# Performance work log

Measured on AMD Instinct MI355X. Metric: run time of the kernel, lower is better.

The kernel has to match this reference:

```python
import jax, jax.numpy as jnp
import numpy as np

N = 8192          # number of nodes
F_IN = 256        # in_features
F_OUT = 128       # out_features


def setup_inputs() -> dict:
    key = jax.random.key(0)
    k1, k2, k3, k4 = jax.random.split(key, 4)
    input = jax.random.normal(k1, (N, F_IN), dtype=jnp.float32)
    adj = jax.random.uniform(k2, (N, N), dtype=jnp.float32)
    stdv = 1.0 / np.sqrt(F_OUT)
    weight = jax.random.uniform(k3, (F_IN, F_OUT), dtype=jnp.float32, minval=-stdv, maxval=stdv)
    bias = jax.random.uniform(k4, (F_OUT,), dtype=jnp.float32, minval=-stdv, maxval=stdv)
    return {"input": input, "adj": adj, "weight": weight, "bias": bias}


def reference(input, adj, weight, bias):
    # support = X @ W  [N, F_OUT]
    support = jnp.matmul(input, weight)
    # Subgraph block decomposition over a node partition is exactly A @ support:
    # block (k,i) computes adj[S_k][:, S_i] @ support[S_i] scatter-added into rows S_k.
    output = jnp.matmul(adj, support)  # [N, F_OUT]
    return output + bias
```

## Files before the change

kernel.cpp:

```cpp
#include <hip/hip_runtime.h>
#include <hip/hip_bf16.h>

#define N_NODES 8192
#define F_IN 256
#define F_OUT 128

#define SPLITK 4
#define KQ (N_NODES / SPLITK)
#define BK 64
#define NT (KQ / BK)
#define ABYTES 16384
#define BBYTES 16384
#define BUFB (ABYTES + BBYTES)

typedef __attribute__((ext_vector_type(4))) float f32x4;
typedef __attribute__((ext_vector_type(8))) short bf16x8;

static __device__ __forceinline__ short bfr(float x) {
    __hip_bfloat16 h = __float2bfloat16(x);
    union { __hip_bfloat16 h; short s; } u; u.h = h;
    return u.s;
}

static __device__ __forceinline__ void gload16(const void* g, void* l) {
    __builtin_amdgcn_global_load_lds(
        (const __attribute__((address_space(1))) unsigned int*)g,
        (__attribute__((address_space(3))) unsigned int*)l, 16, 0, 0);
}

__global__ __launch_bounds__(256) void support_kernel(
        const float* __restrict__ X, const float* __restrict__ W,
        unsigned short* __restrict__ supT) {
    __shared__ float Xs[32][68];
    __shared__ float Ws[64][128];
    const int t = threadIdx.x;
    const int n0 = blockIdx.x * 32;
    const int tc = t & 31;
    const int tr = t >> 5;
    float acc[4][4];
    #pragma unroll
    for (int i = 0; i < 4; ++i)
        #pragma unroll
        for (int j = 0; j < 4; ++j) acc[i][j] = 0.f;

    for (int k0 = 0; k0 < F_IN; k0 += 64) {
        __syncthreads();
        {
            const int r = t >> 3, kc = (t & 7) * 8;
            const float* src = X + (size_t)(n0 + r) * F_IN + k0 + kc;
            f32x4 v0 = *(const f32x4*)src;
            f32x4 v1 = *(const f32x4*)(src + 4);
            *(f32x4*)&Xs[r][kc]     = v0;
            *(f32x4*)&Xs[r][kc + 4] = v1;
        }
        {
            const int col = t & 127, kb = t >> 7;
            #pragma unroll
            for (int i = 0; i < 32; ++i) {
                const int k = kb + i * 2;
                Ws[k][col] = W[(size_t)(k0 + k) * F_OUT + col];
            }
        }
        __syncthreads();
        #pragma unroll 8
        for (int k = 0; k < 64; ++k) {
            const f32x4 b = *(const f32x4*)&Ws[k][tc * 4];
            float a[4];
            #pragma unroll
            for (int i = 0; i < 4; ++i) a[i] = Xs[tr * 4 + i][k];
            #pragma unroll
            for (int i = 0; i < 4; ++i) {
                acc[i][0] += a[i] * b.x; acc[i][1] += a[i] * b.y;
                acc[i][2] += a[i] * b.z; acc[i][3] += a[i] * b.w;
            }
        }
    }
    #pragma unroll
    for (int j = 0; j < 4; ++j) {
        const int col = tc * 4 + j;
        #pragma unroll
        for (int i = 0; i < 4; ++i) {
            supT[(size_t)col * N_NODES + n0 + tr * 4 + i] =
                (unsigned short)bfr(acc[i][j]);
        }
    }
}

__global__ __launch_bounds__(512, 4) void gcn_kernel(
        const float* __restrict__ adj, const unsigned short* __restrict__ supT,
        float* __restrict__ part) {
    __shared__ char lds[2 * BUFB];
    const int t = threadIdx.x;
    const int l = t & 63;
    const int w = t >> 6;
    const int rb = blockIdx.x & 127;
    const int h = blockIdx.x >> 7;
    const int n0 = rb * 64;
    const int k0 = h * KQ;

    const int rA0 = 8 * w + (l >> 4);
    const int rA1 = rA0 + 4;
    const char* gA0 = (const char*)adj
        + ((size_t)(n0 + rA0) * N_NODES + k0) * 4 + (((l & 15) ^ (rA0 & 15)) * 16);
    const char* gA1 = (const char*)adj
        + ((size_t)(n0 + rA1) * N_NODES + k0) * 4 + (((l & 15) ^ (rA1 & 15)) * 16);
    const char* gB0 = (const char*)supT
        + ((size_t)(16 * w + (l >> 3)) * N_NODES + k0) * 2 + (((l & 7) ^ (l >> 3)) * 16);
    const char* gB1 = gB0 + (size_t)8 * N_NODES * 2;

    const int a_d0 = w * 2048;
    const int a_d1 = a_d0 + 1024;
    const int b_d0 = ABYTES + w * 2048;
    const int b_d1 = b_d0 + 1024;

    const int wm = w >> 2, wn = w & 3;
    const int aoff0 = (wm * 32 + (l & 15)) * 256;
    const int aoff1 = aoff0 + 16 * 256;
    const int akey = l & 15;
    const int ac0 = (l >> 4) * 2;
    const int boff0 = ABYTES + (wn * 32 + (l & 15)) * 128;
    const int boff1 = boff0 + 16 * 128;
    const int bkey = l & 7;
    const int cb0 = l >> 4;

    f32x4 acc00 = {0.f,0.f,0.f,0.f}, acc01 = {0.f,0.f,0.f,0.f};
    f32x4 acc10 = {0.f,0.f,0.f,0.f}, acc11 = {0.f,0.f,0.f,0.f};

#define STAGE(BUF) { \
    char* bb = &lds[(BUF) * BUFB]; \
    gload16(gA0, bb + a_d0); \
    gload16(gA1, bb + a_d1); \
    gload16(gB0, bb + b_d0); \
    gload16(gB1, bb + b_d1); \
    gA0 += 256; gA1 += 256; gB0 += 128; gB1 += 128; }

#define FENCE_BARRIER() { \
    asm volatile("s_waitcnt vmcnt(0)" ::: "memory"); \
    __builtin_amdgcn_sched_barrier(0); \
    __builtin_amdgcn_s_barrier(); \
    __builtin_amdgcn_sched_barrier(0); }

    STAGE(0);
    FENCE_BARRIER();

    for (int tt = 0; tt < NT; ++tt) {
        if (tt + 1 < NT) STAGE((tt + 1) & 1);

        const char* buf = &lds[(tt & 1) * BUFB];
        #pragma unroll
        for (int ks = 0; ks < 2; ++ks) {
            const int ca = ks * 8 + ac0;
            f32x4 a0lo = *(const f32x4*)(buf + aoff0 + (((ca    ) ^ akey) * 16));
            f32x4 a0hi = *(const f32x4*)(buf + aoff0 + (((ca + 1) ^ akey) * 16));
            f32x4 a1lo = *(const f32x4*)(buf + aoff1 + (((ca    ) ^ akey) * 16));
            f32x4 a1hi = *(const f32x4*)(buf + aoff1 + (((ca + 1) ^ akey) * 16));
            const int cb = ks * 4 + cb0;
            bf16x8 b0 = *(const bf16x8*)(buf + boff0 + ((cb ^ bkey) * 16));
            bf16x8 b1 = *(const bf16x8*)(buf + boff1 + ((cb ^ bkey) * 16));
            bf16x8 am0, am1;
            am0[0] = bfr(a0lo.x); am0[1] = bfr(a0lo.y);
            am0[2] = bfr(a0lo.z); am0[3] = bfr(a0lo.w);
            am0[4] = bfr(a0hi.x); am0[5] = bfr(a0hi.y);
            am0[6] = bfr(a0hi.z); am0[7] = bfr(a0hi.w);
            am1[0] = bfr(a1lo.x); am1[1] = bfr(a1lo.y);
            am1[2] = bfr(a1lo.z); am1[3] = bfr(a1lo.w);
            am1[4] = bfr(a1hi.x); am1[5] = bfr(a1hi.y);
            am1[6] = bfr(a1hi.z); am1[7] = bfr(a1hi.w);
            acc00 = __builtin_amdgcn_mfma_f32_16x16x32_bf16(am0, b0, acc00, 0, 0, 0);
            acc01 = __builtin_amdgcn_mfma_f32_16x16x32_bf16(am0, b1, acc01, 0, 0, 0);
            acc10 = __builtin_amdgcn_mfma_f32_16x16x32_bf16(am1, b0, acc10, 0, 0, 0);
            acc11 = __builtin_amdgcn_mfma_f32_16x16x32_bf16(am1, b1, acc11, 0, 0, 0);
        }
        FENCE_BARRIER();
    }
#undef STAGE
#undef FENCE_BARRIER

    float* p = part + (size_t)h * N_NODES * F_OUT;
    const int col = wn * 32 + (l & 15);
    const int row0 = n0 + wm * 32 + (l >> 4) * 4;
    #pragma unroll
    for (int i = 0; i < 4; ++i) {
        float* o0 = p + (size_t)(row0 + i) * F_OUT + col;
        float* o1 = p + (size_t)(row0 + i + 16) * F_OUT + col;
        o0[0]  = acc00[i];
        o0[16] = acc01[i];
        o1[0]  = acc10[i];
        o1[16] = acc11[i];
    }
}

__global__ __launch_bounds__(256) void add_kernel(
        const float* __restrict__ part, const float* __restrict__ bias,
        float* __restrict__ out) {
    const int i = blockIdx.x * 256 + threadIdx.x;
    const size_t e = (size_t)i * 8;
    const size_t ps = (size_t)N_NODES * F_OUT;
    f32x4 s0 = *(const f32x4*)(part + e);
    f32x4 s1 = *(const f32x4*)(part + e + 4);
    #pragma unroll
    for (int h = 1; h < SPLITK; ++h) {
        s0 += *(const f32x4*)(part + h * ps + e);
        s1 += *(const f32x4*)(part + h * ps + e + 4);
    }
    const int fb = (i & 15) * 8;
    s0 += *(const f32x4*)(bias + fb);
    s1 += *(const f32x4*)(bias + fb + 4);
    *(f32x4*)(out + e)     = s0;
    *(f32x4*)(out + e + 4) = s1;
}

extern "C" void kernel_launch(void* const* d_in, const int* in_sizes, int n_in,
                              void* d_out, int out_size, void* d_ws, size_t ws_size,
                              hipStream_t stream) {
    const float* input  = (const float*)d_in[0];
    const float* adj    = (const float*)d_in[1];
    const float* weight = (const float*)d_in[2];
    const float* bias   = (const float*)d_in[3];
    float* out = (float*)d_out;
    unsigned short* supT = (unsigned short*)d_ws;
    float* part = (float*)((char*)d_ws + (4u << 20));

    support_kernel<<<N_NODES / 32, 256, 0, stream>>>(input, weight, supT);
    gcn_kernel<<<128 * SPLITK, 512, 0, stream>>>(adj, supT, part);
    add_kernel<<<(N_NODES * F_OUT) / (256 * 8), 256, 0, stream>>>(part, bias, out);
}
```

Measured before the change: 83.66 us.

## Deepen gcn_kernel pipeline to four LDS buffers with smaller K tiles

Halves the K tile to 32 and replaces the double-buffered load/compute loop with a 4-stage ring of LDS buffers. Three stages are prefetched and partial vmcnt waits are used, so global loads stay in flight across iterations instead of draining with vmcnt(0) every tile. The aim is to hide adj streaming latency in this memory-bound GEMM. In exchange there are twice as many barriers per K, and the swizzle and index math has to be redone for the new tile size.

Result: slower. 99.75 us (+19.2%).

```diff
diff --git a/kernel.cpp b/kernel.cpp
--- a/kernel.cpp
+++ b/kernel.cpp
@@ -7,11 +7,12 @@
 
 #define SPLITK 4
 #define KQ (N_NODES / SPLITK)
-#define BK 64
+#define BK 32
 #define NT (KQ / BK)
-#define ABYTES 16384
-#define BBYTES 16384
+#define ABYTES 8192
+#define BBYTES 8192
 #define BUFB (ABYTES + BBYTES)
+#define NBUF 4
 
 typedef __attribute__((ext_vector_type(4))) float f32x4;
 typedef __attribute__((ext_vector_type(8))) short bf16x8;
@@ -89,7 +90,7 @@
 __global__ __launch_bounds__(512, 4) void gcn_kernel(
         const float* __restrict__ adj, const unsigned short* __restrict__ supT,
         float* __restrict__ part) {
-    __shared__ char lds[2 * BUFB];
+    __shared__ char lds[NBUF * BUFB];
     const int t = threadIdx.x;
     const int l = t & 63;
     const int w = t >> 6;
@@ -98,83 +99,74 @@
     const int n0 = rb * 64;
     const int k0 = h * KQ;
 
-    const int rA0 = 8 * w + (l >> 4);
-    const int rA1 = rA0 + 4;
-    const char* gA0 = (const char*)adj
-        + ((size_t)(n0 + rA0) * N_NODES + k0) * 4 + (((l & 15) ^ (rA0 & 15)) * 16);
-    const char* gA1 = (const char*)adj
-        + ((size_t)(n0 + rA1) * N_NODES + k0) * 4 + (((l & 15) ^ (rA1 & 15)) * 16);
-    const char* gB0 = (const char*)supT
-        + ((size_t)(16 * w + (l >> 3)) * N_NODES + k0) * 2 + (((l & 7) ^ (l >> 3)) * 16);
-    const char* gB1 = gB0 + (size_t)8 * N_NODES * 2;
-
-    const int a_d0 = w * 2048;
-    const int a_d1 = a_d0 + 1024;
-    const int b_d0 = ABYTES + w * 2048;
-    const int b_d1 = b_d0 + 1024;
+    const int rA = 8 * w + (l >> 3);
+    const char* gA = (const char*)adj
+        + ((size_t)(n0 + rA) * N_NODES + k0) * 4
+        + (((l & 7) ^ ((l >> 3) & 7)) * 16);
+    const int fB = 16 * w + (l >> 2);
+    const char* gB = (const char*)supT
+        + ((size_t)fB * N_NODES + k0) * 2
+        + (((l & 3) ^ ((l >> 3) & 3)) * 16);
+
+    const int a_d = w * 1024;
+    const int b_d = ABYTES + w * 1024;
 
     const int wm = w >> 2, wn = w & 3;
-    const int aoff0 = (wm * 32 + (l & 15)) * 256;
-    const int aoff1 = aoff0 + 16 * 256;
-    const int akey = l & 15;
-    const int ac0 = (l >> 4) * 2;
-    const int boff0 = ABYTES + (wn * 32 + (l & 15)) * 128;
-    const int boff1 = boff0 + 16 * 128;
-    const int bkey = l & 7;
-    const int cb0 = l >> 4;
+    const int aoff0 = (wm * 32 + (l & 15)) * 128;
+    const int aoff1 = aoff0 + 16 * 128;
+    const int akey = l & 7;
+    const int boff0 = ABYTES + (wn * 32 + (l & 15)) * 64;
+    const int boff1 = boff0 + 16 * 64;
+    const int bkey = (l >> 1) & 3;
+    const int j = l >> 4;
 
     f32x4 acc00 = {0.f,0.f,0.f,0.f}, acc01 = {0.f,0.f,0.f,0.f};
     f32x4 acc10 = {0.f,0.f,0.f,0.f}, acc11 = {0.f,0.f,0.f,0.f};
 
 #define STAGE(BUF) { \
     char* bb = &lds[(BUF) * BUFB]; \
-    gload16(gA0, bb + a_d0); \
-    gload16(gA1, bb + a_d1); \
-    gload16(gB0, bb + b_d0); \
-    gload16(gB1, bb + b_d1); \
-    gA0 += 256; gA1 += 256; gB0 += 128; gB1 += 128; }
-
-#define FENCE_BARRIER() { \
-    asm volatile("s_waitcnt vmcnt(0)" ::: "memory"); \
+    gload16(gA, bb + a_d); \
+    gload16(gB, bb + b_d); \
+    gA += 128; gB += 64; }
+
+#define BODY(TT, WAITIMM, DO_STAGE) { \
+    asm volatile("s_waitcnt vmcnt(" WAITIMM ")" ::: "memory"); \
     __builtin_amdgcn_sched_barrier(0); \
     __builtin_amdgcn_s_barrier(); \
-    __builtin_amdgcn_sched_barrier(0); }
-
-    STAGE(0);
-    FENCE_BARRIER();
-
-    for (int tt = 0; tt < NT; ++tt) {
-        if (tt + 1 < NT) STAGE((tt + 1) & 1);
-
-        const char* buf = &lds[(tt & 1) * BUFB];
-        #pragma unroll
-        for (int ks = 0; ks < 2; ++ks) {
-            const int ca = ks * 8 + ac0;
-            f32x4 a0lo = *(const f32x4*)(buf + aoff0 + (((ca    ) ^ akey) * 16));
-            f32x4 a0hi = *(const f32x4*)(buf + aoff0 + (((ca + 1) ^ akey) * 16));
-            f32x4 a1lo = *(const f32x4*)(buf + aoff1 + (((ca    ) ^ akey) * 16));
-            f32x4 a1hi = *(const f32x4*)(buf + aoff1 + (((ca + 1) ^ akey) * 16));
-            const int cb = ks * 4 + cb0;
-            bf16x8 b0 = *(const bf16x8*)(buf + boff0 + ((cb ^ bkey) * 16));
-            bf16x8 b1 = *(const bf16x8*)(buf + boff1 + ((cb ^ bkey) * 16));
-            bf16x8 am0, am1;
-            am0[0] = bfr(a0lo.x); am0[1] = bfr(a0lo.y);
-            am0[2] = bfr(a0lo.z); am0[3] = bfr(a0lo.w);
-            am0[4] = bfr(a0hi.x); am0[5] = bfr(a0hi.y);
-            am0[6] = bfr(a0hi.z); am0[7] = bfr(a0hi.w);
-            am1[0] = bfr(a1lo.x); am1[1] = bfr(a1lo.y);
-            am1[2] = bfr(a1lo.z); am1[3] = bfr(a1lo.w);
-            am1[4] = bfr(a1hi.x); am1[5] = bfr(a1hi.y);
-            am1[6] = bfr(a1hi.z); am1[7] = bfr(a1hi.w);
-            acc00 = __builtin_amdgcn_mfma_f32_16x16x32_bf16(am0, b0, acc00, 0, 0, 0);
-            acc01 = __builtin_amdgcn_mfma_f32_16x16x32_bf16(am0, b1, acc01, 0, 0, 0);
-            acc10 = __builtin_amdgcn_mfma_f32_16x16x32_bf16(am1, b0, acc10, 0, 0, 0);
-            acc11 = __builtin_amdgcn_mfma_f32_16x16x32_bf16(am1, b1, acc11, 0, 0, 0);
-        }
-        FENCE_BARRIER();
-    }
+    __builtin_amdgcn_sched_barrier(0); \
+    if (DO_STAGE) STAGE(((TT) + 3) & (NBUF - 1)); \
+    const char* buf = &lds[((TT) & (NBUF - 1)) * BUFB]; \
+    f32x4 a0lo = *(const f32x4*)(buf + aoff0 + (((2*j    ) ^ akey) * 16)); \
+    f32x4 a0hi = *(const f32x4*)(buf + aoff0 + (((2*j + 1) ^ akey) * 16)); \
+    f32x4 a1lo = *(const f32x4*)(buf + aoff1 + (((2*j    ) ^ akey) * 16)); \
+    f32x4 a1hi = *(const f32x4*)(buf + aoff1 + (((2*j + 1) ^ akey) * 16)); \
+    bf16x8 b0 = *(const bf16x8*)(buf + boff0 + ((j ^ bkey) * 16)); \
+    bf16x8 b1 = *(const bf16x8*)(buf + boff1 + ((j ^ bkey) * 16)); \
+    bf16x8 am0, am1; \
+    am0[0] = bfr(a0lo.x); am0[1] = bfr(a0lo.y); \
+    am0[2] = bfr(a0lo.z); am0[3] = bfr(a0lo.w); \
+    am0[4] = bfr(a0hi.x); am0[5] = bfr(a0hi.y); \
+    am0[6] = bfr(a0hi.z); am0[7] = bfr(a0hi.w); \
+    am1[0] = bfr(a1lo.x); am1[1] = bfr(a1lo.y); \
+    am1[2] = bfr(a1lo.z); am1[3] = bfr(a1lo.w); \
+    am1[4] = bfr(a1hi.x); am1[5] = bfr(a1hi.y); \
+    am1[6] = bfr(a1hi.z); am1[7] = bfr(a1hi.w); \
+    acc00 = __builtin_amdgcn_mfma_f32_16x16x32_bf16(am0, b0, acc00, 0, 0, 0); \
+    acc01 = __builtin_amdgcn_mfma_f32_16x16x32_bf16(am0, b1, acc01, 0, 0, 0); \
+    acc10 = __builtin_amdgcn_mfma_f32_16x16x32_bf16(am1, b0, acc10, 0, 0, 0); \
+    acc11 = __builtin_amdgcn_mfma_f32_16x16x32_bf16(am1, b1, acc11, 0, 0, 0); }
+
+    STAGE(0); STAGE(1); STAGE(2);
+
+    for (int tt = 0; tt < NT - 3; ++tt) {
+        BODY(tt, "4", 1);
+    }
+    BODY(NT - 3, "4", 0);
+    BODY(NT - 2, "2", 0);
+    BODY(NT - 1, "0", 0);
+
+#undef BODY
 #undef STAGE
-#undef FENCE_BARRIER
 
     float* p = part + (size_t)h * N_NODES * F_OUT;
     const int col = wn * 32 + (l & 15);
```

## Triple-buffer adj tiles and prefetch two stages ahead in GCN kernel

Applied to the files above, without the earlier changes.

Moves the adj (A) operand to a three-buffer LDS ring and keeps supT (B) double-buffered, so A loads are issued two iterations ahead. Each iteration now waits with a partial vmcnt and a single barrier instead of a full drain at the end of the loop. This is meant to hide the latency of the large fp32 adj stream behind MFMA work. It raises LDS use from 64KB to 80KB per block via dynamic shared memory, which may reduce occupancy, and it depends on the vmcnt counts matching the issue order.

New measurement: 87.23 us. 1.04x slower.

```diff
diff --git a/kernel.cpp b/kernel.cpp
--- a/kernel.cpp
+++ b/kernel.cpp
@@ -11,7 +11,7 @@
 #define NT (KQ / BK)
 #define ABYTES 16384
 #define BBYTES 16384
-#define BUFB (ABYTES + BBYTES)
+#define LDS_TOTAL (3 * ABYTES + 2 * BBYTES)
 
 typedef __attribute__((ext_vector_type(4))) float f32x4;
 typedef __attribute__((ext_vector_type(8))) short bf16x8;
@@ -89,7 +89,7 @@
 __global__ __launch_bounds__(512, 4) void gcn_kernel(
         const float* __restrict__ adj, const unsigned short* __restrict__ supT,
         float* __restrict__ part) {
-    __shared__ char lds[2 * BUFB];
+    extern __shared__ char lds[];
     const int t = threadIdx.x;
     const int l = t & 63;
     const int w = t >> 6;
@@ -110,7 +110,7 @@
 
     const int a_d0 = w * 2048;
     const int a_d1 = a_d0 + 1024;
-    const int b_d0 = ABYTES + w * 2048;
+    const int b_d0 = w * 2048;
     const int b_d1 = b_d0 + 1024;
 
     const int wm = w >> 2, wn = w & 3;
@@ -118,7 +118,7 @@
     const int aoff1 = aoff0 + 16 * 256;
     const int akey = l & 15;
     const int ac0 = (l >> 4) * 2;
-    const int boff0 = ABYTES + (wn * 32 + (l & 15)) * 128;
+    const int boff0 = (wn * 32 + (l & 15)) * 128;
     const int boff1 = boff0 + 16 * 128;
     const int bkey = l & 7;
     const int cb0 = l >> 4;
@@ -126,37 +126,46 @@
     f32x4 acc00 = {0.f,0.f,0.f,0.f}, acc01 = {0.f,0.f,0.f,0.f};
     f32x4 acc10 = {0.f,0.f,0.f,0.f}, acc11 = {0.f,0.f,0.f,0.f};
 
-#define STAGE(BUF) { \
-    char* bb = &lds[(BUF) * BUFB]; \
+#define STAGE_A(OFF) { \
+    char* bb = &lds[OFF]; \
     gload16(gA0, bb + a_d0); \
     gload16(gA1, bb + a_d1); \
+    gA0 += 256; gA1 += 256; }
+
+#define STAGE_B(OFF) { \
+    char* bb = &lds[3 * ABYTES + (OFF)]; \
     gload16(gB0, bb + b_d0); \
     gload16(gB1, bb + b_d1); \
-    gA0 += 256; gA1 += 256; gB0 += 128; gB1 += 128; }
-
-#define FENCE_BARRIER() { \
-    asm volatile("s_waitcnt vmcnt(0)" ::: "memory"); \
-    __builtin_amdgcn_sched_barrier(0); \
-    __builtin_amdgcn_s_barrier(); \
-    __builtin_amdgcn_sched_barrier(0); }
-
-    STAGE(0);
-    FENCE_BARRIER();
-
+    gB0 += 128; gB1 += 128; }
+
+    STAGE_B(0);
+    STAGE_A(0);
+    STAGE_A(ABYTES);
+
+    int ai = 0;
+    int bi = 0;
     for (int tt = 0; tt < NT; ++tt) {
-        if (tt + 1 < NT) STAGE((tt + 1) & 1);
-
-        const char* buf = &lds[(tt & 1) * BUFB];
+        if (tt < NT - 1) asm volatile("s_waitcnt vmcnt(2)" ::: "memory");
+        else             asm volatile("s_waitcnt vmcnt(0)" ::: "memory");
+        __builtin_amdgcn_sched_barrier(0);
+        __builtin_amdgcn_s_barrier();
+        __builtin_amdgcn_sched_barrier(0);
+
+        if (tt < NT - 1) STAGE_B((bi ^ 1) * BBYTES);
+        if (tt < NT - 2) { const int as = ai ? ai - 1 : 2; STAGE_A(as * ABYTES); }
+
+        const char* abuf = &lds[ai * ABYTES];
+        const char* bbuf = &lds[3 * ABYTES + bi * BBYTES];
         #pragma unroll
         for (int ks = 0; ks < 2; ++ks) {
             const int ca = ks * 8 + ac0;
-            f32x4 a0lo = *(const f32x4*)(buf + aoff0 + (((ca    ) ^ akey) * 16));
-            f32x4 a0hi = *(const f32x4*)(buf + aoff0 + (((ca + 1) ^ akey) * 16));
-            f32x4 a1lo = *(const f32x4*)(buf + aoff1 + (((ca    ) ^ akey) * 16));
-            f32x4 a1hi = *(const f32x4*)(buf + aoff1 + (((ca + 1) ^ akey) * 16));
+            f32x4 a0lo = *(const f32x4*)(abuf + aoff0 + (((ca    ) ^ akey) * 16));
+            f32x4 a0hi = *(const f32x4*)(abuf + aoff0 + (((ca + 1) ^ akey) * 16));
+            f32x4 a1lo = *(const f32x4*)(abuf + aoff1 + (((ca    ) ^ akey) * 16));
+            f32x4 a1hi = *(const f32x4*)(abuf + aoff1 + (((ca + 1) ^ akey) * 16));
             const int cb = ks * 4 + cb0;
-            bf16x8 b0 = *(const bf16x8*)(buf + boff0 + ((cb ^ bkey) * 16));
-            bf16x8 b1 = *(const bf16x8*)(buf + boff1 + ((cb ^ bkey) * 16));
+            bf16x8 b0 = *(const bf16x8*)(bbuf + boff0 + ((cb ^ bkey) * 16));
+            bf16x8 b1 = *(const bf16x8*)(bbuf + boff1 + ((cb ^ bkey) * 16));
             bf16x8 am0, am1;
             am0[0] = bfr(a0lo.x); am0[1] = bfr(a0lo.y);
             am0[2] = bfr(a0lo.z); am0[3] = bfr(a0lo.w);
@@ -171,10 +180,11 @@
             acc10 = __builtin_amdgcn_mfma_f32_16x16x32_bf16(am1, b0, acc10, 0, 0, 0);
             acc11 = __builtin_amdgcn_mfma_f32_16x16x32_bf16(am1, b1, acc11, 0, 0, 0);
         }
-        FENCE_BARRIER();
-    }
-#undef STAGE
-#undef FENCE_BARRIER
+        ai = (ai == 2) ? 0 : ai + 1;
+        bi ^= 1;
+    }
+#undef STAGE_A
+#undef STAGE_B
 
     float* p = part + (size_t)h * N_NODES * F_OUT;
     const int col = wn * 32 + (l & 15);
@@ -221,7 +231,11 @@
     unsigned short* supT = (unsigned short*)d_ws;
     float* part = (float*)((char*)d_ws + (4u << 20));
 
+    (void)hipFuncSetAttribute((const void*)gcn_kernel,
+                              hipFuncAttributeMaxDynamicSharedMemorySize,
+                              LDS_TOTAL);
+
     support_kernel<<<N_NODES / 32, 256, 0, stream>>>(input, weight, supT);
-    gcn_kernel<<<128 * SPLITK, 512, 0, stream>>>(adj, supT, part);
+    gcn_kernel<<<128 * SPLITK, 512, LDS_TOTAL, stream>>>(adj, supT, part);
     add_kernel<<<(N_NODES * F_OUT) / (256 * 8), 256, 0, stream>>>(part, bias, out);
 }
```

## Fuse split-K reduction and bias into GEMM via atomics; use packed bf16 convert

Applied to the files above, without the earlier changes.

Removes the separate add_kernel and the partial-sum workspace. Each split-K block now atomically adds its tile into a zeroed output, and the h==0 block also adds the bias. The fp32-to-bf16 conversion of adj tiles switches from per-element bfr calls to the packed v_cvt_pk_bf16_f32 instruction, halving the conversion instructions in the inner loop. In exchange it adds a memset, lets the float summation order vary between runs, and relies on atomic throughput to the output.

Measured after the change: 77.73 us. 7.1% less time.

```diff
diff --git a/kernel.cpp b/kernel.cpp
--- a/kernel.cpp
+++ b/kernel.cpp
@@ -15,6 +15,7 @@
 
 typedef __attribute__((ext_vector_type(4))) float f32x4;
 typedef __attribute__((ext_vector_type(8))) short bf16x8;
+typedef __attribute__((ext_vector_type(4))) unsigned int u32x4;
 
 static __device__ __forceinline__ short bfr(float x) {
     __hip_bfloat16 h = __float2bfloat16(x);
@@ -88,7 +89,7 @@
 
 __global__ __launch_bounds__(512, 4) void gcn_kernel(
         const float* __restrict__ adj, const unsigned short* __restrict__ supT,
-        float* __restrict__ part) {
+        const float* __restrict__ bias, float* __restrict__ out) {
     __shared__ char lds[2 * BUFB];
     const int t = threadIdx.x;
     const int l = t & 63;
@@ -125,6 +126,9 @@
 
     f32x4 acc00 = {0.f,0.f,0.f,0.f}, acc01 = {0.f,0.f,0.f,0.f};
     f32x4 acc10 = {0.f,0.f,0.f,0.f}, acc11 = {0.f,0.f,0.f,0.f};
+
+#define PK(dst, a, b) \
+    asm("v_cvt_pk_bf16_f32 %0, %1, %2" : "=v"(dst) : "v"(a), "v"(b))
 
 #define STAGE(BUF) { \
     char* bb = &lds[(BUF) * BUFB]; \
@@ -157,15 +161,13 @@
             const int cb = ks * 4 + cb0;
             bf16x8 b0 = *(const bf16x8*)(buf + boff0 + ((cb ^ bkey) * 16));
             bf16x8 b1 = *(const bf16x8*)(buf + boff1 + ((cb ^ bkey) * 16));
-            bf16x8 am0, am1;
-            am0[0] = bfr(a0lo.x); am0[1] = bfr(a0lo.y);
-            am0[2] = bfr(a0lo.z); am0[3] = bfr(a0lo.w);
-            am0[4] = bfr(a0hi.x); am0[5] = bfr(a0hi.y);
-            am0[6] = bfr(a0hi.z); am0[7] = bfr(a0hi.w);
-            am1[0] = bfr(a1lo.x); am1[1] = bfr(a1lo.y);
-            am1[2] = bfr(a1lo.z); am1[3] = bfr(a1lo.w);
-            am1[4] = bfr(a1hi.x); am1[5] = bfr(a1hi.y);
-            am1[6] = bfr(a1hi.z); am1[7] = bfr(a1hi.w);
+            u32x4 p0, p1;
+            PK(p0.x, a0lo.x, a0lo.y); PK(p0.y, a0lo.z, a0lo.w);
+            PK(p0.z, a0hi.x, a0hi.y); PK(p0.w, a0hi.z, a0hi.w);
+            PK(p1.x, a1lo.x, a1lo.y); PK(p1.y, a1lo.z, a1lo.w);
+            PK(p1.z, a1hi.x, a1hi.y); PK(p1.w, a1hi.z, a1hi.w);
+            bf16x8 am0 = __builtin_bit_cast(bf16x8, p0);
+            bf16x8 am1 = __builtin_bit_cast(bf16x8, p1);
             acc00 = __builtin_amdgcn_mfma_f32_16x16x32_bf16(am0, b0, acc00, 0, 0, 0);
             acc01 = __builtin_amdgcn_mfma_f32_16x16x32_bf16(am0, b1, acc01, 0, 0, 0);
             acc10 = __builtin_amdgcn_mfma_f32_16x16x32_bf16(am1, b0, acc10, 0, 0, 0);
@@ -175,39 +177,21 @@
     }
 #undef STAGE
 #undef FENCE_BARRIER
-
-    float* p = part + (size_t)h * N_NODES * F_OUT;
+#undef PK
+
     const int col = wn * 32 + (l & 15);
     const int row0 = n0 + wm * 32 + (l >> 4) * 4;
+    const float bv0 = (h == 0) ? bias[col]      : 0.0f;
+    const float bv1 = (h == 0) ? bias[col + 16] : 0.0f;
     #pragma unroll
     for (int i = 0; i < 4; ++i) {
-        float* o0 = p + (size_t)(row0 + i) * F_OUT + col;
-        float* o1 = p + (size_t)(row0 + i + 16) * F_OUT + col;
-        o0[0]  = acc00[i];
-        o0[16] = acc01[i];
-        o1[0]  = acc10[i];
-        o1[16] = acc11[i];
-    }
-}
-
-__global__ __launch_bounds__(256) void add_kernel(
-        const float* __restrict__ part, const float* __restrict__ bias,
-        float* __restrict__ out) {
-    const int i = blockIdx.x * 256 + threadIdx.x;
-    const size_t e = (size_t)i * 8;
-    const size_t ps = (size_t)N_NODES * F_OUT;
-    f32x4 s0 = *(const f32x4*)(part + e);
-    f32x4 s1 = *(const f32x4*)(part + e + 4);
-    #pragma unroll
-    for (int h = 1; h < SPLITK; ++h) {
-        s0 += *(const f32x4*)(part + h * ps + e);
-        s1 += *(const f32x4*)(part + h * ps + e + 4);
-    }
-    const int fb = (i & 15) * 8;
-    s0 += *(const f32x4*)(bias + fb);
-    s1 += *(const f32x4*)(bias + fb + 4);
-    *(f32x4*)(out + e)     = s0;
-    *(f32x4*)(out + e + 4) = s1;
+        float* o0 = out + (size_t)(row0 + i) * F_OUT + col;
+        float* o1 = out + (size_t)(row0 + i + 16) * F_OUT + col;
+        unsafeAtomicAdd(&o0[0],  acc00[i] + bv0);
+        unsafeAtomicAdd(&o0[16], acc01[i] + bv1);
+        unsafeAtomicAdd(&o1[0],  acc10[i] + bv0);
+        unsafeAtomicAdd(&o1[16], acc11[i] + bv1);
+    }
 }
 
 extern "C" void kernel_launch(void* const* d_in, const int* in_sizes, int n_in,
@@ -219,9 +203,9 @@
     const float* bias   = (const float*)d_in[3];
     float* out = (float*)d_out;
     unsigned short* supT = (unsigned short*)d_ws;
-    float* part = (float*)((char*)d_ws + (4u << 20));
+
+    hipMemsetAsync(d_out, 0, (size_t)out_size * sizeof(float), stream);
 
     support_kernel<<<N_NODES / 32, 256, 0, stream>>>(input, weight, supT);
-    gcn_kernel<<<128 * SPLITK, 512, 0, stream>>>(adj, supT, part);
-    add_kernel<<<(N_NODES * F_OUT) / (256 * 8), 256, 0, stream>>>(part, bias, out);
-}
+    gcn_kernel<<<128 * SPLITK, 512, 0, stream>>>(adj, supT, bias, out);
+}
```
